# Optimization experiments

Hardware: AMD Instinct MI355X
Metric: run time of the kernel (lower is better)

## Reference

```python
import jax, jax.numpy as jnp
import numpy as np

B, V, P, A, NF = 32, 2048, 64, 8, 128
F = P + A          # concat of transformed features and aggregator weights
DIN = P + 2 * A * F + A  # final cat: orig + expanded_collapsed + agg


def setup_inputs() -> dict:
    key = jax.random.key(0)
    ks = jax.random.split(key, 7)
    s = lambda fan: 1.0 / np.sqrt(fan)
    return {
        "vertices_in": jax.random.normal(ks[0], (B, V, P), dtype=jnp.float32),
        "W1": jax.random.normal(ks[1], (P, P), dtype=jnp.float32) * s(P),
        "b1": jax.random.normal(ks[2], (P,), dtype=jnp.float32) * s(P),
        "W2": jax.random.normal(ks[3], (P, A), dtype=jnp.float32) * s(P),
        "b2": jax.random.normal(ks[4], (A,), dtype=jnp.float32) * s(P),
        "Wout": jax.random.normal(ks[5], (DIN, NF), dtype=jnp.float32) * s(DIN),
        "bout": jax.random.normal(ks[6], (NF,), dtype=jnp.float32) * s(DIN),
    }


def reference(vertices_in, W1, b1, W2, b2, Wout, bout):
    # vertices_in: [B,V,P]
    vi = vertices_in @ W1 + b1                              # [B,V,P]
    agg = jnp.exp(-jnp.abs(vertices_in @ W2 + b2))          # [B,V,A] gauss_of_lin
    feats = jnp.concatenate([vi, agg], axis=-1)             # [B,V,F]
    # edge weights e[b,a,v] = agg[b,v,a]; broadcast multiply then max/mean over V
    prod = jnp.transpose(agg, (0, 2, 1))[:, :, :, None] * feats[:, None, :, :]  # [B,A,V,F]
    mx = jnp.max(prod, axis=2)                              # [B,A,F]
    mn = jnp.mean(prod, axis=2)                             # [B,A,F]
    collapsed = jnp.concatenate([mx, mn], axis=-1)          # [B,A,2F]
    # expand back to vertices: e[b,v,a] * collapsed[b,a,g]
    expanded = agg[:, :, :, None] * collapsed[:, None, :, :]  # [B,V,A,2F]
    expanded = expanded.reshape(B, V, A * 2 * F)
    x = jnp.concatenate([vertices_in, expanded, agg], axis=-1)  # [B,V,DIN]
    return jnp.tanh(x @ Wout + bout)                        # [B,V,NF]
```

## Files before the change

kernel.cpp:

```cpp
#include <hip/hip_runtime.h>
#include <math.h>

#define BB 32
#define VV 2048
#define PP 64
#define AA 8
#define NFF 128
#define FF 72
#define TWOF 144

__global__ __launch_bounds__(256) void k1_feats(
        const float* __restrict__ x,
        const float* __restrict__ W1, const float* __restrict__ b1,
        const float* __restrict__ W2, const float* __restrict__ b2,
        float* __restrict__ featsT, float* __restrict__ agg) {
    const int b = blockIdx.y;
    const int v = blockIdx.x * 256 + threadIdx.x;

    float xs[64];
    const float4* xp = reinterpret_cast<const float4*>(x + ((size_t)b * VV + v) * PP);
    #pragma unroll
    for (int i = 0; i < 16; ++i) {
        float4 t = xp[i];
        xs[4 * i + 0] = t.x; xs[4 * i + 1] = t.y; xs[4 * i + 2] = t.z; xs[4 * i + 3] = t.w;
    }

    #pragma unroll 1
    for (int c = 0; c < 16; ++c) {
        float4 acc = make_float4(b1[4 * c + 0], b1[4 * c + 1], b1[4 * c + 2], b1[4 * c + 3]);
        #pragma unroll
        for (int p = 0; p < 64; ++p) {
            const float4 w = *reinterpret_cast<const float4*>(&W1[p * 64 + 4 * c]);
            const float xv = xs[p];
            acc.x += xv * w.x; acc.y += xv * w.y; acc.z += xv * w.z; acc.w += xv * w.w;
        }
        float* fr = featsT + ((size_t)b * FF + 4 * c) * VV + v;
        fr[0 * VV] = acc.x; fr[1 * VV] = acc.y; fr[2 * VV] = acc.z; fr[3 * VV] = acc.w;
    }

    float ex[8];
    #pragma unroll 1
    for (int cc = 0; cc < 2; ++cc) {
        float4 acc = make_float4(b2[4 * cc + 0], b2[4 * cc + 1], b2[4 * cc + 2], b2[4 * cc + 3]);
        #pragma unroll
        for (int p = 0; p < 64; ++p) {
            const float4 w = *reinterpret_cast<const float4*>(&W2[p * 8 + 4 * cc]);
            const float xv = xs[p];
            acc.x += xv * w.x; acc.y += xv * w.y; acc.z += xv * w.z; acc.w += xv * w.w;
        }
        acc.x = __expf(-fabsf(acc.x));
        acc.y = __expf(-fabsf(acc.y));
        acc.z = __expf(-fabsf(acc.z));
        acc.w = __expf(-fabsf(acc.w));
        float* fr = featsT + ((size_t)b * FF + 64 + 4 * cc) * VV + v;
        fr[0 * VV] = acc.x; fr[1 * VV] = acc.y; fr[2 * VV] = acc.z; fr[3 * VV] = acc.w;
        ex[4 * cc + 0] = acc.x; ex[4 * cc + 1] = acc.y; ex[4 * cc + 2] = acc.z; ex[4 * cc + 3] = acc.w;
    }

    float4* ap = reinterpret_cast<float4*>(agg + ((size_t)b * VV + v) * AA);
    ap[0] = make_float4(ex[0], ex[1], ex[2], ex[3]);
    ap[1] = make_float4(ex[4], ex[5], ex[6], ex[7]);
}

__global__ __launch_bounds__(256) void k2_reduce(
        const float* __restrict__ featsT, const float* __restrict__ agg,
        float* __restrict__ collapsed) {
    const int fg = blockIdx.x;
    const int b  = blockIdx.y;
    const int f0 = fg * 4;
    const int t  = threadIdx.x;
    const int wave = t >> 6, lane = t & 63;

    __shared__ float redm[4][32];
    __shared__ float reds[4][32];

    float pmax[4][8], psum[4][8];
    #pragma unroll
    for (int j = 0; j < 4; ++j)
        #pragma unroll
        for (int a = 0; a < 8; ++a) { pmax[j][a] = -INFINITY; psum[j][a] = 0.0f; }

    for (int i = 0; i < 8; ++i) {
        const int v = i * 256 + t;
        const float4* ep = reinterpret_cast<const float4*>(agg + ((size_t)b * VV + v) * AA);
        const float4 e0 = ep[0], e1 = ep[1];
        float e[8];
        e[0] = e0.x; e[1] = e0.y; e[2] = e0.z; e[3] = e0.w;
        e[4] = e1.x; e[5] = e1.y; e[6] = e1.z; e[7] = e1.w;
        #pragma unroll
        for (int j = 0; j < 4; ++j) {
            const float fv = featsT[((size_t)b * FF + f0 + j) * VV + v];
            #pragma unroll
            for (int a = 0; a < 8; ++a) {
                const float pr = e[a] * fv;
                pmax[j][a] = fmaxf(pmax[j][a], pr);
                psum[j][a] += pr;
            }
        }
    }

    #pragma unroll
    for (int j = 0; j < 4; ++j) {
        #pragma unroll
        for (int a = 0; a < 8; ++a) {
            float m = pmax[j][a];
            float s = psum[j][a];
            #pragma unroll
            for (int d = 1; d < 64; d <<= 1) {
                m = fmaxf(m, __shfl_xor(m, d));
                s += __shfl_xor(s, d);
            }
            if (lane == 0) { redm[wave][j * 8 + a] = m; reds[wave][j * 8 + a] = s; }
        }
    }
    __syncthreads();

    if (t < 32) {
        const int j = t >> 3, a = t & 7;
        float m = redm[0][t], s = reds[0][t];
        #pragma unroll
        for (int w = 1; w < 4; ++w) { m = fmaxf(m, redm[w][t]); s += reds[w][t]; }
        float* cr = collapsed + ((size_t)b * AA + a) * TWOF;
        cr[f0 + j]      = m;
        cr[FF + f0 + j] = s * (1.0f / (float)VV);
    }
}

__global__ __launch_bounds__(256) void k2b_mprime(
        const float* __restrict__ collapsed, const float* __restrict__ Wout,
        float* __restrict__ Mp) {
    const int a = blockIdx.x, b = blockIdx.y;
    const int t = threadIdx.x;
    const int nf = t & 127, gh = t >> 7;
    __shared__ float part[2][128];

    const float* col  = collapsed + ((size_t)b * AA + a) * TWOF;
    const float* Wexp = Wout + (size_t)(64 + a * TWOF) * NFF;

    float acc = 0.0f;
    const int g0 = gh * 72;
    #pragma unroll 8
    for (int g = g0; g < g0 + 72; ++g)
        acc += col[g] * Wexp[(size_t)g * NFF + nf];
    part[gh][nf] = acc;
    __syncthreads();

    if (t < 128) {
        float r = part[0][t] + part[1][t] + Wout[(size_t)(1216 + a) * NFF + t];
        Mp[((size_t)b * AA + a) * NFF + t] = r;
    }
}

__device__ __forceinline__ float fast_tanh(float z) {
    const float e = __expf(2.0f * z);
    return 1.0f - 2.0f / (e + 1.0f);
}

__global__ __launch_bounds__(256) void k3_out(
        const float* __restrict__ x, const float* __restrict__ agg,
        const float* __restrict__ Mp, const float* __restrict__ Wout,
        const float* __restrict__ bout, float* __restrict__ out) {
    const int b = blockIdx.y;
    const int v = blockIdx.x * 256 + threadIdx.x;

    float xs[64];
    const float4* xp = reinterpret_cast<const float4*>(x + ((size_t)b * VV + v) * PP);
    #pragma unroll
    for (int i = 0; i < 16; ++i) {
        float4 t = xp[i];
        xs[4 * i + 0] = t.x; xs[4 * i + 1] = t.y; xs[4 * i + 2] = t.z; xs[4 * i + 3] = t.w;
    }
    float e[8];
    const float4* ep = reinterpret_cast<const float4*>(agg + ((size_t)b * VV + v) * AA);
    {
        const float4 e0 = ep[0], e1 = ep[1];
        e[0] = e0.x; e[1] = e0.y; e[2] = e0.z; e[3] = e0.w;
        e[4] = e1.x; e[5] = e1.y; e[6] = e1.z; e[7] = e1.w;
    }

    const float* Mpb = Mp + (size_t)b * AA * NFF;
    float4* op = reinterpret_cast<float4*>(out + ((size_t)b * VV + v) * NFF);

    #pragma unroll 1
    for (int c = 0; c < 32; ++c) {
        float4 acc = make_float4(bout[4 * c + 0], bout[4 * c + 1],
                                 bout[4 * c + 2], bout[4 * c + 3]);
        #pragma unroll
        for (int p = 0; p < 64; ++p) {
            const float4 w = *reinterpret_cast<const float4*>(&Wout[(size_t)p * NFF + 4 * c]);
            const float xv = xs[p];
            acc.x += xv * w.x; acc.y += xv * w.y; acc.z += xv * w.z; acc.w += xv * w.w;
        }
        #pragma unroll
        for (int a = 0; a < 8; ++a) {
            const float4 w = *reinterpret_cast<const float4*>(&Mpb[(size_t)a * NFF + 4 * c]);
            const float ea = e[a];
            acc.x += ea * w.x; acc.y += ea * w.y; acc.z += ea * w.z; acc.w += ea * w.w;
        }
        acc.x = fast_tanh(acc.x); acc.y = fast_tanh(acc.y);
        acc.z = fast_tanh(acc.z); acc.w = fast_tanh(acc.w);
        op[c] = acc;
    }
}

extern "C" void kernel_launch(void* const* d_in, const int* in_sizes, int n_in,
                              void* d_out, int out_size, void* d_ws, size_t ws_size,
                              hipStream_t stream) {
    const float* x    = (const float*)d_in[0];
    const float* W1   = (const float*)d_in[1];
    const float* b1   = (const float*)d_in[2];
    const float* W2   = (const float*)d_in[3];
    const float* b2   = (const float*)d_in[4];
    const float* Wout = (const float*)d_in[5];
    const float* bout = (const float*)d_in[6];
    float* out = (float*)d_out;

    float* ws     = (float*)d_ws;
    float* featsT = ws;
    float* agg    = featsT + (size_t)BB * FF * VV;
    float* coll   = agg + (size_t)BB * VV * AA;
    float* Mp     = coll + (size_t)BB * AA * TWOF;

    k1_feats<<<dim3(8, 32), dim3(256), 0, stream>>>(x, W1, b1, W2, b2, featsT, agg);
    k2_reduce<<<dim3(18, 32), dim3(256), 0, stream>>>(featsT, agg, coll);
    k2b_mprime<<<dim3(8, 32), dim3(256), 0, stream>>>(coll, Wout, Mp);
    k3_out<<<dim3(8, 32), dim3(256), 0, stream>>>(x, agg, Mp, Wout, bout, out);
}
```

Measured before the change: 194.1 us.

## Split output columns across waves in k1 and k3 to raise parallelism

```diff
diff --git a/kernel.cpp b/kernel.cpp
--- a/kernel.cpp
+++ b/kernel.cpp
@@ -14,52 +14,53 @@
         const float* __restrict__ W1, const float* __restrict__ b1,
         const float* __restrict__ W2, const float* __restrict__ b2,
         float* __restrict__ featsT, float* __restrict__ agg) {
-    const int b = blockIdx.y;
-    const int v = blockIdx.x * 256 + threadIdx.x;
+    const int b    = blockIdx.y;
+    const int t    = threadIdx.x;
+    const int w    = __builtin_amdgcn_readfirstlane(t >> 6);
+    const int lane = t & 63;
+    const int v    = blockIdx.x * 64 + lane;
 
     float xs[64];
     const float4* xp = reinterpret_cast<const float4*>(x + ((size_t)b * VV + v) * PP);
     #pragma unroll
     for (int i = 0; i < 16; ++i) {
-        float4 t = xp[i];
-        xs[4 * i + 0] = t.x; xs[4 * i + 1] = t.y; xs[4 * i + 2] = t.z; xs[4 * i + 3] = t.w;
+        float4 t4 = xp[i];
+        xs[4 * i + 0] = t4.x; xs[4 * i + 1] = t4.y; xs[4 * i + 2] = t4.z; xs[4 * i + 3] = t4.w;
     }
 
     #pragma unroll 1
-    for (int c = 0; c < 16; ++c) {
-        float4 acc = make_float4(b1[4 * c + 0], b1[4 * c + 1], b1[4 * c + 2], b1[4 * c + 3]);
-        #pragma unroll
-        for (int p = 0; p < 64; ++p) {
-            const float4 w = *reinterpret_cast<const float4*>(&W1[p * 64 + 4 * c]);
-            const float xv = xs[p];
-            acc.x += xv * w.x; acc.y += xv * w.y; acc.z += xv * w.z; acc.w += xv * w.w;
-        }
-        float* fr = featsT + ((size_t)b * FF + 4 * c) * VV + v;
+    for (int k = 0; k < 5; ++k) {
+        const int c = w + 4 * k;
+        if (c >= 18) break;
+        const int f0 = 4 * c;
+        float4 acc;
+        if (c < 16) {
+            acc = make_float4(b1[f0 + 0], b1[f0 + 1], b1[f0 + 2], b1[f0 + 3]);
+            #pragma unroll
+            for (int p = 0; p < 64; ++p) {
+                const float4 wt = *reinterpret_cast<const float4*>(&W1[p * 64 + f0]);
+                const float xv = xs[p];
+                acc.x += xv * wt.x; acc.y += xv * wt.y; acc.z += xv * wt.z; acc.w += xv * wt.w;
+            }
+        } else {
+            const int a0 = f0 - 64;
+            acc = make_float4(b2[a0 + 0], b2[a0 + 1], b2[a0 + 2], b2[a0 + 3]);
+            #pragma unroll
+            for (int p = 0; p < 64; ++p) {
+                const float4 wt = *reinterpret_cast<const float4*>(&W2[p * 8 + a0]);
+                const float xv = xs[p];
+                acc.x += xv * wt.x; acc.y += xv * wt.y; acc.z += xv * wt.z; acc.w += xv * wt.w;
+            }
+            acc.x = __expf(-fabsf(acc.x));
+            acc.y = __expf(-fabsf(acc.y));
+            acc.z = __expf(-fabsf(acc.z));
+            acc.w = __expf(-fabsf(acc.w));
+            float4* ap = reinterpret_cast<float4*>(agg + ((size_t)b * VV + v) * AA);
+            ap[c - 16] = acc;
+        }
+        float* fr = featsT + ((size_t)b * FF + f0) * VV + v;
         fr[0 * VV] = acc.x; fr[1 * VV] = acc.y; fr[2 * VV] = acc.z; fr[3 * VV] = acc.w;
     }
-
-    float ex[8];
-    #pragma unroll 1
-    for (int cc = 0; cc < 2; ++cc) {
-        float4 acc = make_float4(b2[4 * cc + 0], b2[4 * cc + 1], b2[4 * cc + 2], b2[4 * cc + 3]);
-        #pragma unroll
-        for (int p = 0; p < 64; ++p) {
-            const float4 w = *reinterpret_cast<const float4*>(&W2[p * 8 + 4 * cc]);
-            const float xv = xs[p];
-            acc.x += xv * w.x; acc.y += xv * w.y; acc.z += xv * w.z; acc.w += xv * w.w;
-        }
-        acc.x = __expf(-fabsf(acc.x));
-        acc.y = __expf(-fabsf(acc.y));
-        acc.z = __expf(-fabsf(acc.z));
-        acc.w = __expf(-fabsf(acc.w));
-        float* fr = featsT + ((size_t)b * FF + 64 + 4 * cc) * VV + v;
-        fr[0 * VV] = acc.x; fr[1 * VV] = acc.y; fr[2 * VV] = acc.z; fr[3 * VV] = acc.w;
-        ex[4 * cc + 0] = acc.x; ex[4 * cc + 1] = acc.y; ex[4 * cc + 2] = acc.z; ex[4 * cc + 3] = acc.w;
-    }
-
-    float4* ap = reinterpret_cast<float4*>(agg + ((size_t)b * VV + v) * AA);
-    ap[0] = make_float4(ex[0], ex[1], ex[2], ex[3]);
-    ap[1] = make_float4(ex[4], ex[5], ex[6], ex[7]);
 }
 
 __global__ __launch_bounds__(256) void k2_reduce(
@@ -160,15 +161,19 @@
         const float* __restrict__ x, const float* __restrict__ agg,
         const float* __restrict__ Mp, const float* __restrict__ Wout,
         const float* __restrict__ bout, float* __restrict__ out) {
-    const int b = blockIdx.y;
-    const int v = blockIdx.x * 256 + threadIdx.x;
+    const int b    = blockIdx.y;
+    const int t    = threadIdx.x;
+    const int q    = __builtin_amdgcn_readfirstlane(t >> 6);
+    const int lane = t & 63;
+    const int v    = blockIdx.x * 64 + lane;
+    const int n0   = q * 32;
 
     float xs[64];
     const float4* xp = reinterpret_cast<const float4*>(x + ((size_t)b * VV + v) * PP);
     #pragma unroll
     for (int i = 0; i < 16; ++i) {
-        float4 t = xp[i];
-        xs[4 * i + 0] = t.x; xs[4 * i + 1] = t.y; xs[4 * i + 2] = t.z; xs[4 * i + 3] = t.w;
+        float4 t4 = xp[i];
+        xs[4 * i + 0] = t4.x; xs[4 * i + 1] = t4.y; xs[4 * i + 2] = t4.z; xs[4 * i + 3] = t4.w;
     }
     float e[8];
     const float4* ep = reinterpret_cast<const float4*>(agg + ((size_t)b * VV + v) * AA);
@@ -178,28 +183,30 @@
         e[4] = e1.x; e[5] = e1.y; e[6] = e1.z; e[7] = e1.w;
     }
 
-    const float* Mpb = Mp + (size_t)b * AA * NFF;
-    float4* op = reinterpret_cast<float4*>(out + ((size_t)b * VV + v) * NFF);
+    const float* Wq  = Wout + n0;
+    const float* Mpq = Mp + (size_t)b * AA * NFF + n0;
+    const float* bq  = bout + n0;
+    float* op = out + ((size_t)b * VV + v) * NFF + n0;
 
     #pragma unroll 1
-    for (int c = 0; c < 32; ++c) {
-        float4 acc = make_float4(bout[4 * c + 0], bout[4 * c + 1],
-                                 bout[4 * c + 2], bout[4 * c + 3]);
+    for (int cc = 0; cc < 8; ++cc) {
+        float4 acc = make_float4(bq[4 * cc + 0], bq[4 * cc + 1],
+                                 bq[4 * cc + 2], bq[4 * cc + 3]);
         #pragma unroll
         for (int p = 0; p < 64; ++p) {
-            const float4 w = *reinterpret_cast<const float4*>(&Wout[(size_t)p * NFF + 4 * c]);
+            const float4 wt = *reinterpret_cast<const float4*>(&Wq[(size_t)p * NFF + 4 * cc]);
             const float xv = xs[p];
-            acc.x += xv * w.x; acc.y += xv * w.y; acc.z += xv * w.z; acc.w += xv * w.w;
+            acc.x += xv * wt.x; acc.y += xv * wt.y; acc.z += xv * wt.z; acc.w += xv * wt.w;
         }
         #pragma unroll
         for (int a = 0; a < 8; ++a) {
-            const float4 w = *reinterpret_cast<const float4*>(&Mpb[(size_t)a * NFF + 4 * c]);
+            const float4 wt = *reinterpret_cast<const float4*>(&Mpq[(size_t)a * NFF + 4 * cc]);
             const float ea = e[a];
-            acc.x += ea * w.x; acc.y += ea * w.y; acc.z += ea * w.z; acc.w += ea * w.w;
+            acc.x += ea * wt.x; acc.y += ea * wt.y; acc.z += ea * wt.z; acc.w += ea * wt.w;
         }
         acc.x = fast_tanh(acc.x); acc.y = fast_tanh(acc.y);
         acc.z = fast_tanh(acc.z); acc.w = fast_tanh(acc.w);
-        op[c] = acc;
+        *reinterpret_cast<float4*>(&op[4 * cc]) = acc;
     }
 }
 
@@ -221,8 +228,8 @@
     float* coll   = agg + (size_t)BB * VV * AA;
     float* Mp     = coll + (size_t)BB * AA * TWOF;
 
-    k1_feats<<<dim3(8, 32), dim3(256), 0, stream>>>(x, W1, b1, W2, b2, featsT, agg);
+    k1_feats<<<dim3(32, 32), dim3(256), 0, stream>>>(x, W1, b1, W2, b2, featsT, agg);
     k2_reduce<<<dim3(18, 32), dim3(256), 0, stream>>>(featsT, agg, coll);
     k2b_mprime<<<dim3(8, 32), dim3(256), 0, stream>>>(coll, Wout, Mp);
-    k3_out<<<dim3(8, 32), dim3(256), 0, stream>>>(x, agg, Mp, Wout, bout, out);
-}
+    k3_out<<<dim3(32, 32), dim3(256), 0, stream>>>(x, agg, Mp, Wout, bout, out);
+}
```

Result: faster. 169.9 us (-12.5%).
